# Kernel optimization log

Measured on AMD Instinct MI355X. Metric: run time of the kernel, lower is better.

The kernel has to match this reference:

```python
import jax, jax.numpy as jnp
import numpy as np


def setup_inputs() -> dict:
    key = jax.random.key(0)
    k1, k2, k3, k4, k5 = jax.random.split(key, 5)
    B, S, IN, OUT, R = 4, 2048, 4096, 4096, 16
    x = jax.random.normal(k1, (B, S, IN), dtype=jnp.float32)
    weight = jax.random.normal(k2, (OUT, IN), dtype=jnp.float32) * 0.02
    bias = jax.random.normal(k3, (OUT,), dtype=jnp.float32) * 0.02
    lora_A = jax.random.normal(k4, (R, IN), dtype=jnp.float32) * 0.02
    lora_B = jax.random.normal(k5, (OUT, R), dtype=jnp.float32) * 0.02
    return {"x": x, "weight": weight, "bias": bias, "lora_A": lora_A, "lora_B": lora_B}


def reference(x, weight, bias, lora_A, lora_B):
    # HiRA (Linear path): out = x @ (W * (1 + A^T B^T)^T)^T + bias
    # prod_AB[i, o] = sum_r A[r, i] * B[o, r]; adapted_weight[o, i] = W[o, i] * (prod_AB + 1)[i, o]
    prod_AB = jnp.einsum('ri,or->io', lora_A, lora_B) + 1.0       # [in, out]
    adapted_weight = weight * prod_AB.T                            # [out, in]
    # F.linear: x @ adapted_weight^T + bias
    return jnp.einsum('bsi,oi->bso', x, adapted_weight) + bias
```

## Files before the change

### kernel.cpp

```cpp
#include <hip/hip_runtime.h>
#include <hip/hip_bf16.h>
#include <stdint.h>

#define M_DIM 8192
#define N_DIM 4096
#define K_DIM 4096
#define R_DIM 16

typedef __bf16 bf16x8 __attribute__((ext_vector_type(8)));
typedef float f32x4 __attribute__((ext_vector_type(4)));
typedef unsigned short u16x8 __attribute__((ext_vector_type(8)));

#define AS1(p) ((const __attribute__((address_space(1))) void*)(p))
#define AS3(p) ((__attribute__((address_space(3))) void*)(p))

#define BAR() do { asm volatile("" ::: "memory"); __builtin_amdgcn_s_barrier(); asm volatile("" ::: "memory"); } while (0)
#define VMCNT2() asm volatile("s_waitcnt vmcnt(2)" ::: "memory")
#define VMCNT0() asm volatile("s_waitcnt vmcnt(0)" ::: "memory")
#define VMCNT8() asm volatile("s_waitcnt vmcnt(8)" ::: "memory")

__device__ __forceinline__ unsigned short f2bf(float f) {
  unsigned u = __builtin_bit_cast(unsigned, f);
  u += 0x7FFFu + ((u >> 16) & 1u);
  return (unsigned short)(u >> 16);
}

#define CVT_BLOCKS 4096
__global__ void __launch_bounds__(256) prep_kernel(
    const float* __restrict__ x, const float* __restrict__ W,
    const float* __restrict__ lA, const float* __restrict__ lB,
    unsigned short* __restrict__ xb, unsigned short* __restrict__ awb) {
  __shared__ float Asub[16 * 512];
  __shared__ float Bsub[32 * 16];
  const int tid = threadIdx.x;

  if (blockIdx.x < 1024) {
    const int i0 = (blockIdx.x & 7) * 512;
    const int o0 = (blockIdx.x >> 3) * 32;
    for (int idx = tid; idx < 16 * 512; idx += 256) {
      int r = idx >> 9, i = idx & 511;
      Asub[idx] = lA[r * K_DIM + i0 + i];
    }
    for (int idx = tid; idx < 32 * 16; idx += 256) {
      int o = idx >> 4, r = idx & 15;
      Bsub[idx] = lB[(o0 + o) * R_DIM + r];
    }
    __syncthreads();
    for (int idx = tid; idx < 32 * 512; idx += 256) {
      int o = idx >> 9, i = idx & 511;
      float s = 1.0f;
#pragma unroll
      for (int r = 0; r < 16; ++r) s += Asub[r * 512 + i] * Bsub[o * 16 + r];
      size_t g = (size_t)(o0 + o) * K_DIM + i0 + i;
      awb[g] = f2bf(W[g] * s);
    }
  } else {
    const long total = (long)M_DIM * K_DIM;
    long i = ((long)(blockIdx.x - 1024) * 256 + tid) * 8;
    const long stride = (long)CVT_BLOCKS * 256 * 8;
    for (; i < total; i += stride) {
      const float4* p = (const float4*)(x + i);
      float4 f0 = p[0], f1 = p[1];
      u16x8 v;
      v[0] = f2bf(f0.x); v[1] = f2bf(f0.y); v[2] = f2bf(f0.z); v[3] = f2bf(f0.w);
      v[4] = f2bf(f1.x); v[5] = f2bf(f1.y); v[6] = f2bf(f1.z); v[7] = f2bf(f1.w);
      *(u16x8*)(xb + i) = v;
    }
  }
}

__global__ void __launch_bounds__(512, 2) gemm_kernel(
    const unsigned short* __restrict__ Ag,
    const unsigned short* __restrict__ Bg,
    const float* __restrict__ bias,
    float* __restrict__ out) {
  __shared__ __attribute__((aligned(16))) unsigned short LDS[2 * 32768];

  const int nwg = gridDim.x;
  const int q8 = nwg >> 3;
  const int wg = blockIdx.x;
  const int swz = (wg & 7) * q8 + (wg >> 3);
  const int tiles_n = N_DIM / 256;
  const int brow = (swz / tiles_n) * 256;
  const int bcol = (swz % tiles_n) * 256;

  const int tid = threadIdx.x;
  const int lane = tid & 63;
  const int w = tid >> 6;
  const int wr = w >> 2, wc = w & 3;
  const int fr = lane & 15;
  const int kq = (lane >> 4) << 3;

  const int rr = lane >> 2;
  const int cc = ((lane & 1) << 3) | ((((lane >> 1) ^ (lane >> 5)) & 1) << 4);
  const int c_sw = ((w & 1) << 5) | cc;
  const int rbase = ((w >> 1) << 4) + rr;

  const unsigned short* srcA[2][2];
#pragma unroll
  for (int h = 0; h < 2; ++h)
#pragma unroll
    for (int q = 0; q < 2; ++q)
      srcA[h][q] = Ag + (size_t)(brow + h * 128 + q * 64 + rbase) * K_DIM + c_sw;
  const long long bdelta = (long long)(Bg - Ag) + (long long)(bcol - brow) * K_DIM;

  auto stageA = [&](int buf, int h, int kt) {
#pragma unroll
    for (int q = 0; q < 2; ++q)
      __builtin_amdgcn_global_load_lds(AS1(srcA[h][q] + (size_t)kt * 64),
          AS3(&LDS[buf * 32768 + h * 8192 + q * 4096 + w * 512]), 16, 0, 0);
  };
  auto stageB = [&](int buf, int h, int kt) {
#pragma unroll
    for (int q = 0; q < 2; ++q)
      __builtin_amdgcn_global_load_lds(AS1(srcA[h][q] + bdelta + (size_t)kt * 64),
          AS3(&LDS[buf * 32768 + 16384 + h * 8192 + q * 4096 + w * 512]), 16, 0, 0);
  };

  const int rdsw = ((fr << 6) | (kq << 1)) ^ ((fr & 8) << 2);
  auto lda = [&](int buf, int m, int kk) -> bf16x8 {
    return *(const bf16x8*)((const char*)LDS +
        (buf * 65536 + wr * 16384 + (m * 2 + kk) * 1024 + rdsw));
  };
  auto ldb = [&](int buf, int n, int kk) -> bf16x8 {
    return *(const bf16x8*)((const char*)LDS +
        (buf * 65536 + 32768 + (wc >> 1) * 16384 +
         (((wc & 1) * 4 + n) * 2 + kk) * 1024 + rdsw));
  };

  f32x4 acc[8][4] = {};
  bf16x8 a[2][4];
  bf16x8 blo[2][2], bhi[2][2];

  auto read_a = [&](int buf, int mg) {
#pragma unroll
    for (int kk = 0; kk < 2; ++kk)
#pragma unroll
      for (int mi = 0; mi < 4; ++mi)
        a[kk][mi] = lda(buf, mg + mi, kk);
  };
  auto read_blo = [&](int buf) {
#pragma unroll
    for (int kk = 0; kk < 2; ++kk)
#pragma unroll
      for (int ni = 0; ni < 2; ++ni)
        blo[kk][ni] = ldb(buf, ni, kk);
  };
  auto read_bhi = [&](int buf) {
#pragma unroll
    for (int kk = 0; kk < 2; ++kk)
#pragma unroll
      for (int ni = 0; ni < 2; ++ni)
        bhi[kk][ni] = ldb(buf, 2 + ni, kk);
  };
  auto mma_b = [&](bf16x8 (&bb)[2][2], int am, int an) {
#pragma unroll
    for (int mi = 0; mi < 4; ++mi)
#pragma unroll
      for (int ni = 0; ni < 2; ++ni)
#pragma unroll
        for (int kk = 0; kk < 2; ++kk)
          acc[am + mi][an + ni] = __builtin_amdgcn_mfma_f32_16x16x32_bf16(
              a[kk][mi], bb[kk][ni], acc[am + mi][an + ni], 0, 0, 0);
  };

  auto tile_body = [&](int t, int buf, bool g2, bool gr) {
    const int nxbuf = buf ^ 1;
    if (g2) stageB(buf, 0, t + 2);
    __builtin_amdgcn_s_setprio(1);
    mma_b(blo, 0, 0); mma_b(bhi, 0, 2);
    __builtin_amdgcn_s_setprio(0);
    read_a(buf, 4);
    if (g2) { VMCNT2(); } else { VMCNT0(); }
    BAR();
    if (g2) { stageB(buf, 1, t + 2); stageA(buf, 0, t + 2); stageA(buf, 1, t + 2); }
    __builtin_amdgcn_s_setprio(1);
    mma_b(bhi, 4, 2); mma_b(blo, 4, 0);
    __builtin_amdgcn_s_setprio(0);
    if (gr) { read_bhi(nxbuf); read_a(nxbuf, 0); read_blo(nxbuf); }
    BAR();
  };

  stageB(0, 0, 0); stageB(0, 1, 0); stageA(0, 0, 0); stageA(0, 1, 0);
  stageB(1, 0, 1); stageB(1, 1, 1); stageA(1, 0, 1); stageA(1, 1, 1);
  VMCNT8();
  BAR();
  read_bhi(0); read_a(0, 0); read_blo(0);

#pragma unroll 1
  for (int i = 0; i < 32; ++i) {
    const bool more = (i < 31);
    tile_body(2 * i,     0, more, true);
    tile_body(2 * i + 1, 1, more, more);
  }

  const int fq = (lane >> 4) * 4;
#pragma unroll
  for (int n = 0; n < 4; ++n) {
    const int col = bcol + wc * 64 + n * 16 + fr;
    const float bb = bias[col];
#pragma unroll
    for (int m = 0; m < 8; ++m) {
      const int row = brow + wr * 128 + m * 16 + fq;
      f32x4 v = acc[m][n];
#pragma unroll
      for (int j = 0; j < 4; ++j)
        out[(size_t)(row + j) * N_DIM + col] = v[j] + bb;
    }
  }
}

extern "C" void kernel_launch(void* const* d_in, const int* in_sizes, int n_in,
                              void* d_out, int out_size, void* d_ws, size_t ws_size,
                              hipStream_t stream) {
  const float* x    = (const float*)d_in[0];
  const float* W    = (const float*)d_in[1];
  const float* bias = (const float*)d_in[2];
  const float* lA   = (const float*)d_in[3];
  const float* lB   = (const float*)d_in[4];
  float* out = (float*)d_out;

  unsigned short* xb  = (unsigned short*)d_ws;
  unsigned short* awb = xb + (size_t)M_DIM * K_DIM;

  prep_kernel<<<1024 + CVT_BLOCKS, 256, 0, stream>>>(x, W, lA, lB, xb, awb);
  gemm_kernel<<<(M_DIM / 256) * (N_DIM / 256), 512, 0, stream>>>(xb, awb, bias, out);
}
```

Baseline: 297.1 us.

## Switch GEMM to 32x32x16 MFMA with new LDS tile layout

Replaces the 16x16x32 bf16 MFMA tiling with 32x32x16 MFMA instructions, so each wave holds a 4x2 grid of 32x32 accumulators instead of 8x4 16x16 ones. The global-to-LDS staging layout and the LDS read offsets are redesigned so that each wave loads contiguous 32-row blocks, and the half-tile read/compute schedule is simplified. The goal is fewer MFMA issues and fewer LDS reads per FLOP. The new layout drops the previous XOR swizzle, which may bring LDS bank conflicts, and the epilogue store pattern changes.

```diff
diff --git a/kernel.cpp b/kernel.cpp
--- a/kernel.cpp
+++ b/kernel.cpp
@@ -6,9 +6,10 @@
 #define N_DIM 4096
 #define K_DIM 4096
 #define R_DIM 16
+#define NT    (K_DIM / 64)
 
 typedef __bf16 bf16x8 __attribute__((ext_vector_type(8)));
-typedef float f32x4 __attribute__((ext_vector_type(4)));
+typedef float f32x16 __attribute__((ext_vector_type(16)));
 typedef unsigned short u16x8 __attribute__((ext_vector_type(8)));
 
 #define AS1(p) ((const __attribute__((address_space(1))) void*)(p))
@@ -74,7 +75,7 @@
     const unsigned short* __restrict__ Bg,
     const float* __restrict__ bias,
     float* __restrict__ out) {
-  __shared__ __attribute__((aligned(16))) unsigned short LDS[2 * 32768];
+  __shared__ __attribute__((aligned(16))) char LDSc[2 * 65536];
 
   const int nwg = gridDim.x;
   const int q8 = nwg >> 3;
@@ -88,104 +89,74 @@
   const int lane = tid & 63;
   const int w = tid >> 6;
   const int wr = w >> 2, wc = w & 3;
-  const int fr = lane & 15;
-  const int kq = (lane >> 4) << 3;
-
-  const int rr = lane >> 2;
-  const int cc = ((lane & 1) << 3) | ((((lane >> 1) ^ (lane >> 5)) & 1) << 4);
-  const int c_sw = ((w & 1) << 5) | cc;
-  const int rbase = ((w >> 1) << 4) + rr;
-
-  const unsigned short* srcA[2][2];
-#pragma unroll
-  for (int h = 0; h < 2; ++h)
-#pragma unroll
-    for (int q = 0; q < 2; ++q)
-      srcA[h][q] = Ag + (size_t)(brow + h * 128 + q * 64 + rbase) * K_DIM + c_sw;
-  const long long bdelta = (long long)(Bg - Ag) + (long long)(bcol - brow) * K_DIM;
-
-  auto stageA = [&](int buf, int h, int kt) {
-#pragma unroll
-    for (int q = 0; q < 2; ++q)
-      __builtin_amdgcn_global_load_lds(AS1(srcA[h][q] + (size_t)kt * 64),
-          AS3(&LDS[buf * 32768 + h * 8192 + q * 4096 + w * 512]), 16, 0, 0);
-  };
-  auto stageB = [&](int buf, int h, int kt) {
-#pragma unroll
-    for (int q = 0; q < 2; ++q)
-      __builtin_amdgcn_global_load_lds(AS1(srcA[h][q] + bdelta + (size_t)kt * 64),
-          AS3(&LDS[buf * 32768 + 16384 + h * 8192 + q * 4096 + w * 512]), 16, 0, 0);
-  };
-
-  const int rdsw = ((fr << 6) | (kq << 1)) ^ ((fr & 8) << 2);
-  auto lda = [&](int buf, int m, int kk) -> bf16x8 {
-    return *(const bf16x8*)((const char*)LDS +
-        (buf * 65536 + wr * 16384 + (m * 2 + kk) * 1024 + rdsw));
-  };
-  auto ldb = [&](int buf, int n, int kk) -> bf16x8 {
-    return *(const bf16x8*)((const char*)LDS +
-        (buf * 65536 + 32768 + (wc >> 1) * 16384 +
-         (((wc & 1) * 4 + n) * 2 + kk) * 1024 + rdsw));
-  };
-
-  f32x4 acc[8][4] = {};
-  bf16x8 a[2][4];
-  bf16x8 blo[2][2], bhi[2][2];
-
-  auto read_a = [&](int buf, int mg) {
-#pragma unroll
-    for (int kk = 0; kk < 2; ++kk)
+
+  const int grow = ((lane >> 1) & 1) * 16 + (lane >> 2);
+  const int gcol = (lane & 1) * 8;
+
+  const unsigned short* srcAbase = Ag + (size_t)(brow + w * 32 + grow) * K_DIM + gcol;
+  const unsigned short* srcBbase = Bg + (size_t)(bcol + w * 32 + grow) * K_DIM + gcol;
+
+  auto stageA4 = [&](int buf, int kt) {
+#pragma unroll
+    for (int j = 0; j < 4; ++j)
+      __builtin_amdgcn_global_load_lds(AS1(srcAbase + (size_t)kt * 64 + j * 16),
+          AS3(LDSc + buf * 65536 + w * 4096 + j * 1024), 16, 0, 0);
+  };
+  auto stageB2 = [&](int buf, int kt, int j0) {
+#pragma unroll
+    for (int j = 0; j < 2; ++j)
+      __builtin_amdgcn_global_load_lds(AS1(srcBbase + (size_t)kt * 64 + (j0 + j) * 16),
+          AS3(LDSc + buf * 65536 + 32768 + w * 4096 + (j0 + j) * 1024), 16, 0, 0);
+  };
+
+  const int loff = (lane & 15) * 64 + (((lane >> 4) & 1) * 2 + (lane >> 5)) * 16;
+
+  f32x16 acc[4][2] = {};
+  bf16x8 a[2][4], b[2][2];
+
+  auto read_half = [&](int buf, int half) {
+#pragma unroll
+    for (int j = 0; j < 2; ++j)
 #pragma unroll
       for (int mi = 0; mi < 4; ++mi)
-        a[kk][mi] = lda(buf, mg + mi, kk);
-  };
-  auto read_blo = [&](int buf) {
-#pragma unroll
-    for (int kk = 0; kk < 2; ++kk)
+        a[j][mi] = *(const bf16x8*)(LDSc + buf * 65536 +
+            (wr * 4 + mi) * 4096 + (half * 2 + j) * 1024 + loff);
+#pragma unroll
+    for (int j = 0; j < 2; ++j)
 #pragma unroll
       for (int ni = 0; ni < 2; ++ni)
-        blo[kk][ni] = ldb(buf, ni, kk);
-  };
-  auto read_bhi = [&](int buf) {
-#pragma unroll
-    for (int kk = 0; kk < 2; ++kk)
+        b[j][ni] = *(const bf16x8*)(LDSc + buf * 65536 + 32768 +
+            (wc * 2 + ni) * 4096 + (half * 2 + j) * 1024 + loff);
+  };
+  auto mma_half = [&]() {
+#pragma unroll
+    for (int mi = 0; mi < 4; ++mi)
 #pragma unroll
       for (int ni = 0; ni < 2; ++ni)
-        bhi[kk][ni] = ldb(buf, 2 + ni, kk);
-  };
-  auto mma_b = [&](bf16x8 (&bb)[2][2], int am, int an) {
-#pragma unroll
-    for (int mi = 0; mi < 4; ++mi)
-#pragma unroll
-      for (int ni = 0; ni < 2; ++ni)
-#pragma unroll
-        for (int kk = 0; kk < 2; ++kk)
-          acc[am + mi][an + ni] = __builtin_amdgcn_mfma_f32_16x16x32_bf16(
-              a[kk][mi], bb[kk][ni], acc[am + mi][an + ni], 0, 0, 0);
+#pragma unroll
+        for (int j = 0; j < 2; ++j)
+          acc[mi][ni] = __builtin_amdgcn_mfma_f32_32x32x16_bf16(
+              a[j][mi], b[j][ni], acc[mi][ni], 0, 0, 0);
   };
 
   auto tile_body = [&](int t, int buf, bool g2, bool gr) {
     const int nxbuf = buf ^ 1;
-    if (g2) stageB(buf, 0, t + 2);
-    __builtin_amdgcn_s_setprio(1);
-    mma_b(blo, 0, 0); mma_b(bhi, 0, 2);
-    __builtin_amdgcn_s_setprio(0);
-    read_a(buf, 4);
+    if (g2) stageB2(buf, t + 2, 0);
+    __builtin_amdgcn_s_setprio(1); mma_half(); __builtin_amdgcn_s_setprio(0);
+    read_half(buf, 1);
     if (g2) { VMCNT2(); } else { VMCNT0(); }
     BAR();
-    if (g2) { stageB(buf, 1, t + 2); stageA(buf, 0, t + 2); stageA(buf, 1, t + 2); }
-    __builtin_amdgcn_s_setprio(1);
-    mma_b(bhi, 4, 2); mma_b(blo, 4, 0);
-    __builtin_amdgcn_s_setprio(0);
-    if (gr) { read_bhi(nxbuf); read_a(nxbuf, 0); read_blo(nxbuf); }
+    if (g2) { stageB2(buf, t + 2, 2); stageA4(buf, t + 2); }
+    __builtin_amdgcn_s_setprio(1); mma_half(); __builtin_amdgcn_s_setprio(0);
+    if (gr) read_half(nxbuf, 0);
     BAR();
   };
 
-  stageB(0, 0, 0); stageB(0, 1, 0); stageA(0, 0, 0); stageA(0, 1, 0);
-  stageB(1, 0, 1); stageB(1, 1, 1); stageA(1, 0, 1); stageA(1, 1, 1);
+  stageB2(0, 0, 0); stageB2(0, 0, 2); stageA4(0, 0);
+  stageB2(1, 1, 0); stageB2(1, 1, 2); stageA4(1, 1);
   VMCNT8();
   BAR();
-  read_bhi(0); read_a(0, 0); read_blo(0);
+  read_half(0, 0);
 
 #pragma unroll 1
   for (int i = 0; i < 32; ++i) {
@@ -194,18 +165,21 @@
     tile_body(2 * i + 1, 1, more, more);
   }
 
-  const int fq = (lane >> 4) * 4;
-#pragma unroll
-  for (int n = 0; n < 4; ++n) {
-    const int col = bcol + wc * 64 + n * 16 + fr;
+  const int c32 = lane & 31;
+  const int r4 = (lane >> 5) * 4;
+#pragma unroll
+  for (int ni = 0; ni < 2; ++ni) {
+    const int col = bcol + wc * 64 + ni * 32 + c32;
     const float bb = bias[col];
 #pragma unroll
-    for (int m = 0; m < 8; ++m) {
-      const int row = brow + wr * 128 + m * 16 + fq;
-      f32x4 v = acc[m][n];
-#pragma unroll
-      for (int j = 0; j < 4; ++j)
-        out[(size_t)(row + j) * N_DIM + col] = v[j] + bb;
+    for (int mi = 0; mi < 4; ++mi) {
+      const int rowbase = brow + wr * 128 + mi * 32 + r4;
+      f32x16 v = acc[mi][ni];
+#pragma unroll
+      for (int reg = 0; reg < 16; ++reg) {
+        const int row = rowbase + (reg & 3) + 8 * (reg >> 2);
+        out[(size_t)row * N_DIM + col] = v[reg] + bb;
+      }
     }
   }
 }
```

Result: slower. 332.4 us (+11.9%).
